# Optimization experiments

Hardware: AMD Instinct MI355X
Metric: run time of the kernel (lower is better)

Reference implementation:

```python
import jax, jax.numpy as jnp
import numpy as np

N, D, H, E = 4096, 512, 8, 131072
DH = D // H
BN_EPS = 1e-5


def setup_inputs() -> dict:
    key = jax.random.key(0)
    ks = jax.random.split(key, 12)
    def w(k, shape):
        return jax.random.normal(k, shape, dtype=jnp.float32) * 0.02
    return {
        'x': jax.random.normal(ks[0], (N, D), dtype=jnp.float32),
        'edge_index': jax.random.randint(ks[1], (2, E), 0, N),
        'edge_attr': jax.random.normal(ks[2], (E, D), dtype=jnp.float32),
        # GINE MLP: Linear(D,D) -> ReLU -> Linear(D,D)  (torch layout [out,in])
        'w_gin1': w(ks[3], (D, D)), 'b_gin1': jnp.zeros((D,), jnp.float32),
        'w_gin2': w(ks[4], (D, D)), 'b_gin2': jnp.zeros((D,), jnp.float32),
        # MultiheadAttention in/out projections
        'w_qkv': w(ks[5], (3 * D, D)), 'b_qkv': jnp.zeros((3 * D,), jnp.float32),
        'w_o': w(ks[6], (D, D)), 'b_o': jnp.zeros((D,), jnp.float32),
        # BatchNorm affine params
        'bn1l_g': jnp.ones((D,), jnp.float32), 'bn1l_b': jnp.zeros((D,), jnp.float32),
        'bn1a_g': jnp.ones((D,), jnp.float32), 'bn1a_b': jnp.zeros((D,), jnp.float32),
        # FFN: D -> 2D -> D
        'w_ff1': w(ks[7], (2 * D, D)), 'b_ff1': jnp.zeros((2 * D,), jnp.float32),
        'w_ff2': w(ks[8], (D, 2 * D)), 'b_ff2': jnp.zeros((D,), jnp.float32),
        'bn2_g': jnp.ones((D,), jnp.float32), 'bn2_b': jnp.zeros((D,), jnp.float32),
    }


def _bn(x, g, b):
    # BatchNorm1d in training mode: batch statistics over the node dim
    m = jnp.mean(x, axis=0)
    v = jnp.var(x, axis=0)
    return (x - m) * jax.lax.rsqrt(v + BN_EPS) * g + b


def _forward(x, edge_index, edge_attr,
             w_gin1, b_gin1, w_gin2, b_gin2,
             w_qkv, b_qkv, w_o, b_o,
             bn1l_g, bn1l_b, bn1a_g, bn1a_b,
             w_ff1, b_ff1, w_ff2, b_ff2, bn2_g, bn2_b):
    h_in = x
    src, dst = edge_index[0], edge_index[1]
    # --- local GINEConv: nn((1+eps)*x + sum_j relu(x_j + e_ji)), eps=0 ---
    msg = jax.nn.relu(x[src] + edge_attr)                       # [E, D]
    agg = jax.ops.segment_sum(msg, dst, num_segments=N)         # [N, D]
    gin_h = x + agg
    h_local = jax.nn.relu(gin_h @ w_gin1.T + b_gin1) @ w_gin2.T + b_gin2
    h_local = _bn(h_in + h_local, bn1l_g, bn1l_b)               # residual + BN
    # --- global multi-head self-attention over all nodes (single graph) ---
    qkv = x @ w_qkv.T + b_qkv                                   # [N, 3D]
    q, k, v = jnp.split(qkv, 3, axis=-1)
    q = q.reshape(N, H, DH).transpose(1, 0, 2)                  # [H, N, DH]
    k = k.reshape(N, H, DH).transpose(1, 0, 2)
    v = v.reshape(N, H, DH).transpose(1, 0, 2)
    scores = jnp.einsum('hnd,hmd->hnm', q, k) / np.float32(np.sqrt(DH))
    attn = jax.nn.softmax(scores, axis=-1)                      # [H, N, N]
    o = jnp.einsum('hnm,hmd->hnd', attn, v).transpose(1, 0, 2).reshape(N, D)
    h_attn = _bn(h_in + (o @ w_o.T + b_o), bn1a_g, bn1a_b)
    # --- combine branches + FFN block ---
    h = h_local + h_attn
    h = h + (jax.nn.relu(h @ w_ff1.T + b_ff1) @ w_ff2.T + b_ff2)
    return _bn(h, bn2_g, bn2_b)


def reference(x, edge_index, edge_attr,
              w_gin1, b_gin1, w_gin2, b_gin2,
              w_qkv, b_qkv, w_o, b_o,
              bn1l_g, bn1l_b, bn1a_g, bn1a_b,
              w_ff1, b_ff1, w_ff2, b_ff2, bn2_g, bn2_b):
    return _forward(x, edge_index, edge_attr,
                    w_gin1, b_gin1, w_gin2, b_gin2,
                    w_qkv, b_qkv, w_o, b_o,
                    bn1l_g, bn1l_b, bn1a_g, bn1a_b,
                    w_ff1, b_ff1, w_ff2, b_ff2, bn2_g, bn2_b)
```

## Files before the change

### kernel.cpp

```cpp
#include <hip/hip_runtime.h>

#define Nn 4096
#define Dd 512
#define Hh 8
#define Ee 131072
#define DEGCAP 96

typedef __attribute__((ext_vector_type(8))) short short8v;
typedef __attribute__((ext_vector_type(4))) short short4v;
typedef __attribute__((ext_vector_type(4))) float f32x4v;
typedef __attribute__((ext_vector_type(4))) unsigned short ushort4v;

__device__ __forceinline__ float bf2f(unsigned short u) {
    return __uint_as_float(((unsigned int)u) << 16);
}
__device__ __forceinline__ unsigned short f2bf(float f) {
    unsigned int u = __float_as_uint(f);
    return (unsigned short)((u + 0x7fff + ((u >> 16) & 1)) >> 16);
}
__device__ __forceinline__ void gl_lds16(const void* g, void* l) {
    __builtin_amdgcn_global_load_lds((const __attribute__((address_space(1))) void*)g,
                                     (__attribute__((address_space(3))) void*)l, 16, 0, 0);
}

struct CastJobs {
    const float* src[6];
    unsigned short* dst[6];
    int start[7];
    int* cnt;
    float* stats;
};

__global__ __launch_bounds__(256) void cast_multi(CastJobs cj) {
    int gid = blockIdx.x * 256 + threadIdx.x;
    if (gid < 4096) cj.cnt[gid] = 0;
    if (gid < 6144) cj.stats[gid] = 0.f;
    int b = blockIdx.x;
    int j = 0;
    while (b >= cj.start[j + 1]) j++;
    int off = (b - cj.start[j]) * 1024 + threadIdx.x * 4;
    f32x4v v = *(const f32x4v*)(cj.src[j] + off);
    ushort4v o;
    o.x = f2bf(v.x); o.y = f2bf(v.y); o.z = f2bf(v.z); o.w = f2bf(v.w);
    *(ushort4v*)(cj.dst[j] + off) = o;
}

__global__ __launch_bounds__(256) void edge_scatter(const int* __restrict__ ei,
                                                    int* __restrict__ cnt,
                                                    int* __restrict__ eidx) {
    int e = blockIdx.x * 256 + threadIdx.x;
    int d = ei[Ee + e];
    int pos = atomicAdd(&cnt[d], 1);
    if (pos < DEGCAP) eidx[d * DEGCAP + pos] = e;
}

__global__ __launch_bounds__(256) void gine_gather(const float* __restrict__ x,
                                                   const int* __restrict__ ei,
                                                   const float* __restrict__ ea,
                                                   const int* __restrict__ cnt,
                                                   const int* __restrict__ eidx,
                                                   unsigned short* __restrict__ gh,
                                                   unsigned short* __restrict__ xb) {
    __shared__ int se[DEGCAP];
    __shared__ int ss[DEGCAP];
    __shared__ float part[512];
    const int node = blockIdx.x;
    const int t = threadIdx.x;
    const int deg = min(cnt[node], DEGCAP);
    const int tc = t & 127, ep = t >> 7;

    if (t < deg) {
        int e = eidx[node * DEGCAP + t];
        se[t] = e;
        ss[t] = ei[e];
    }
    __syncthreads();

    f32x4v acc = {0.f, 0.f, 0.f, 0.f};
    int k = ep;
    while (k + 2 < deg) {
        int e0 = se[k], s0 = ss[k];
        int e1 = se[k + 2], s1 = ss[k + 2];
        f32x4v ev0 = *(const f32x4v*)(ea + (size_t)e0 * Dd + tc * 4);
        f32x4v xv0 = *(const f32x4v*)(x + (size_t)s0 * Dd + tc * 4);
        f32x4v ev1 = *(const f32x4v*)(ea + (size_t)e1 * Dd + tc * 4);
        f32x4v xv1 = *(const f32x4v*)(x + (size_t)s1 * Dd + tc * 4);
#pragma unroll
        for (int i = 0; i < 4; i++) {
            acc[i] += fmaxf(xv0[i] + ev0[i], 0.f);
            acc[i] += fmaxf(xv1[i] + ev1[i], 0.f);
        }
        k += 4;
    }
    if (k < deg) {
        int e0 = se[k], s0 = ss[k];
        f32x4v ev0 = *(const f32x4v*)(ea + (size_t)e0 * Dd + tc * 4);
        f32x4v xv0 = *(const f32x4v*)(x + (size_t)s0 * Dd + tc * 4);
#pragma unroll
        for (int i = 0; i < 4; i++) acc[i] += fmaxf(xv0[i] + ev0[i], 0.f);
    }

    if (ep) *(f32x4v*)&part[tc * 4] = acc;
    __syncthreads();
    if (!ep) {
        f32x4v o = *(const f32x4v*)&part[tc * 4];
        f32x4v xd = *(const f32x4v*)(x + (size_t)node * Dd + tc * 4);
        ushort4v ov, xv;
#pragma unroll
        for (int i = 0; i < 4; i++) {
            ov[i] = f2bf(xd[i] + acc[i] + o[i]);
            xv[i] = f2bf(xd[i]);
        }
        *(ushort4v*)(gh + (size_t)node * Dd + tc * 4) = ov;
        *(ushort4v*)(xb + (size_t)node * Dd + tc * 4) = xv;
    }
}

template <int K, int MB, bool RELU, bool OUTBF16, bool ADDRES, bool SXADD, int SOFF>
__global__ __launch_bounds__(256) void gemm_bt(const short* __restrict__ A,
                                               const short* __restrict__ B,
                                               const float* __restrict__ bias,
                                               const float* __restrict__ res,
                                               void* __restrict__ outp, int Nc,
                                               const float* __restrict__ sx,
                                               float* __restrict__ stats) {
    constexpr int BM = MB * 32;
    __shared__ alignas(16) short lA[BM * 32];
    __shared__ alignas(16) short lB[128 * 32];
    const int t = threadIdx.x;
    const int lane = t & 63, w = t >> 6;
    const int wr = w >> 1, wc = w & 1;
    const int l15 = lane & 15, lhi = lane >> 4;
    const int m0 = blockIdx.y * BM, n0 = blockIdx.x * 128;
    f32x4v acc[MB][4] = {};
    const int c0 = t, c1 = t + 256;

    for (int k0 = 0; k0 < K; k0 += 32) {
        __syncthreads();
        gl_lds16(A + (size_t)(m0 + (c0 >> 2)) * K + k0 + (c0 & 3) * 8, (char*)lA + c0 * 16);
        if constexpr (MB == 4)
            gl_lds16(A + (size_t)(m0 + (c1 >> 2)) * K + k0 + (c1 & 3) * 8, (char*)lA + c1 * 16);
        gl_lds16(B + (size_t)(n0 + (c0 >> 2)) * K + k0 + (c0 & 3) * 8, (char*)lB + c0 * 16);
        gl_lds16(B + (size_t)(n0 + (c1 >> 2)) * K + k0 + (c1 & 3) * 8, (char*)lB + c1 * 16);
        __syncthreads();
        short8v af[MB], bf[4];
#pragma unroll
        for (int m = 0; m < MB; m++)
            af[m] = *(const short8v*)&lA[(wr * (MB * 16) + m * 16 + l15) * 32 + lhi * 8];
#pragma unroll
        for (int n = 0; n < 4; n++)
            bf[n] = *(const short8v*)&lB[(wc * 64 + n * 16 + l15) * 32 + lhi * 8];
#pragma unroll
        for (int m = 0; m < MB; m++)
#pragma unroll
            for (int n = 0; n < 4; n++)
                acc[m][n] = __builtin_amdgcn_mfma_f32_16x16x32_bf16(af[m], bf[n], acc[m][n], 0, 0, 0);
    }

    float csum[4] = {0.f, 0.f, 0.f, 0.f}, cssq[4] = {0.f, 0.f, 0.f, 0.f};

#pragma unroll
    for (int m = 0; m < MB; m++)
#pragma unroll
        for (int n = 0; n < 4; n++)
#pragma unroll
            for (int j = 0; j < 4; j++) {
                int col = n0 + wc * 64 + n * 16 + l15;
                int row = m0 + wr * (MB * 16) + m * 16 + lhi * 4 + j;
                size_t idx = (size_t)row * Nc + col;
                float v = acc[m][n][j] + bias[col];
                if (RELU) v = fmaxf(v, 0.f);
                if (ADDRES) v += res[idx];
                if constexpr (SOFF >= 0) {
                    float a = SXADD ? (sx[idx] + v) : v;
                    csum[n] += a;
                    cssq[n] += a * a;
                }
                if (OUTBF16)
                    ((unsigned short*)outp)[idx] = f2bf(v);
                else
                    ((float*)outp)[idx] = v;
            }

    if constexpr (SOFF >= 0) {
        __shared__ float sst[256];
        sst[t] = 0.f;
        __syncthreads();
#pragma unroll
        for (int n = 0; n < 4; n++) {
            float s = csum[n], q = cssq[n];
            s += __shfl_xor(s, 16); s += __shfl_xor(s, 32);
            q += __shfl_xor(q, 16); q += __shfl_xor(q, 32);
            if (lhi == 0) {
                int c = wc * 64 + n * 16 + l15;
                atomicAdd(&sst[c * 2], s);
                atomicAdd(&sst[c * 2 + 1], q);
            }
        }
        __syncthreads();
        int c = t >> 1;
        atomicAdd(&stats[SOFF + (t & 1) * 512 + n0 + c], sst[t]);
    }
}

__global__ __launch_bounds__(256) void attn_fwd(const short* __restrict__ qkv,
                                                unsigned short* __restrict__ opart0,
                                                unsigned short* __restrict__ opart1,
                                                float* __restrict__ lsum) {
    __shared__ alignas(16) short lK[2][64 * 64];
    __shared__ alignas(16) short lV[2][4 * 64 * 16];
    __shared__ alignas(16) short lP[4 * 2 * 16 * 64];
    const int t = threadIdx.x, lane = t & 63, w = t >> 6;
    const int h = blockIdx.y >> 1, half = blockIdx.y & 1;
    const int kvbase = half * 2048;
    const int qw = blockIdx.x * 128 + w * 32;
    const int l15 = lane & 15, lhi = lane >> 4;
    const int ksw = l15 & 7;
    const int qs3 = (l15 >> 1) & 7;
    unsigned short* __restrict__ opart = half ? opart1 : opart0;

    short* pP = lP + w * 2048;

    short8v qf[2][2];
#pragma unroll
    for (int g = 0; g < 2; g++)
#pragma unroll
        for (int kk = 0; kk < 2; kk++)
            qf[g][kk] = *(const short8v*)&qkv[(size_t)(qw + g * 16 + l15) * 1536 + h * 64 + kk * 32 + lhi * 8];

    f32x4v oacc[2][4] = {};
    float lrow[2] = {0.f, 0.f};
    const float SC2 = 0.125f * 1.44269504f;

    int kidx[4][2];
#pragma unroll
    for (int r = 0; r < 4; r++)
#pragma unroll
        for (int kk = 0; kk < 2; kk++)
            kidx[r][kk] = (l15 + r * 16) * 64 + (((kk * 4 + lhi) ^ ksw) * 8);

    int pw_idx[4], prd_idx[2];
#pragma unroll
    for (int c2 = 0; c2 < 4; c2++)
        pw_idx[c2] = l15 * 64 + (((c2 * 2 + (lhi >> 1)) ^ qs3) * 8) + ((lhi & 1) * 4);
#pragma unroll
    for (int c = 0; c < 2; c++)
        prd_idx[c] = l15 * 64 + (((c * 4 + lhi) ^ qs3) * 8);

    unsigned vbase0 = (unsigned)(unsigned long long)&lV[0][0] + lhi * 256 + l15 * 2;

    auto stage = [&](int kt, int b) {
        int kv0 = kvbase + kt * 64;
#pragma unroll
        for (int i = 0; i < 2; i++) {
            int row = (t >> 3) + 32 * i;
            gl_lds16(qkv + (size_t)(kv0 + row) * 1536 + 512 + h * 64 + ((t & 7) ^ ((t >> 3) & 7)) * 8,
                     (char*)&lK[b][0] + t * 16 + i * 4096);
        }
#pragma unroll
        for (int i = 0; i < 2; i++) {
            int db = (t >> 7) + 2 * i;
            int kv = (t >> 1) & 63;
            int dh_in = (t & 1) * 8;
            gl_lds16(qkv + (size_t)(kv0 + kv) * 1536 + 1024 + h * 64 + db * 16 + dh_in,
                     (char*)&lV[b][0] + t * 16 + i * 4096);
        }
    };

    stage(0, 0);
    __syncthreads();

    for (int kt = 0; kt < 32; kt++) {
        const int b = kt & 1;
        if (kt + 1 < 32) stage(kt + 1, b ^ 1);

        const short* Kb = &lK[b][0];
        const unsigned vbase = vbase0 + b * 8192;

        f32x4v s0[4] = {}, s1[4] = {};
        __builtin_amdgcn_s_setprio(1);
#pragma unroll
        for (int r = 0; r < 4; r++) {
            short8v k0 = *(const short8v*)&Kb[kidx[r][0]];
            short8v k1 = *(const short8v*)&Kb[kidx[r][1]];
            s0[r] = __builtin_amdgcn_mfma_f32_16x16x32_bf16(k0, qf[0][0], s0[r], 0, 0, 0);
            s0[r] = __builtin_amdgcn_mfma_f32_16x16x32_bf16(k1, qf[0][1], s0[r], 0, 0, 0);
            s1[r] = __builtin_amdgcn_mfma_f32_16x16x32_bf16(k0, qf[1][0], s1[r], 0, 0, 0);
            s1[r] = __builtin_amdgcn_mfma_f32_16x16x32_bf16(k1, qf[1][1], s1[r], 0, 0, 0);
        }
        __builtin_amdgcn_s_setprio(0);

#pragma unroll
        for (int g = 0; g < 2; g++) {
            f32x4v* s = g ? s1 : s0;
            float p[16];
            float rs = 0.f;
#pragma unroll
            for (int r = 0; r < 4; r++)
#pragma unroll
                for (int j = 0; j < 4; j++) {
                    float e = exp2f(fmaf(s[r][j], SC2, -4.f));
                    p[r * 4 + j] = e;
                    rs += e;
                }
            rs += __shfl_xor(rs, 16);
            rs += __shfl_xor(rs, 32);
            lrow[g] += rs;

            short* pPg = pP + g * 1024;
#pragma unroll
            for (int c2 = 0; c2 < 4; c2++) {
                short4v pk;
#pragma unroll
                for (int j = 0; j < 4; j++) pk[j] = (short)f2bf(p[c2 * 4 + j]);
                *(short4v*)&pPg[pw_idx[c2]] = pk;
            }
        }
        asm volatile("" ::: "memory");

        short8v pf[2][2];
#pragma unroll
        for (int g = 0; g < 2; g++)
#pragma unroll
            for (int c = 0; c < 2; c++)
                pf[g][c] = *(const short8v*)&pP[g * 1024 + prd_idx[c]];

        short4v v00a, v00b, v01a, v01b, v10a, v10b, v11a, v11b;
        short4v v20a, v20b, v21a, v21b, v30a, v30b, v31a, v31b;
        asm volatile("ds_read_b64_tr_b16 %0, %1" : "=v"(v00a) : "v"(vbase));
        asm volatile("ds_read_b64_tr_b16 %0, %1 offset:128" : "=v"(v00b) : "v"(vbase));
        asm volatile("ds_read_b64_tr_b16 %0, %1 offset:1024" : "=v"(v01a) : "v"(vbase));
        asm volatile("ds_read_b64_tr_b16 %0, %1 offset:1152" : "=v"(v01b) : "v"(vbase));
        asm volatile("ds_read_b64_tr_b16 %0, %1 offset:2048" : "=v"(v10a) : "v"(vbase));
        asm volatile("ds_read_b64_tr_b16 %0, %1 offset:2176" : "=v"(v10b) : "v"(vbase));
        asm volatile("ds_read_b64_tr_b16 %0, %1 offset:3072" : "=v"(v11a) : "v"(vbase));
        asm volatile("ds_read_b64_tr_b16 %0, %1 offset:3200" : "=v"(v11b) : "v"(vbase));
        asm volatile("ds_read_b64_tr_b16 %0, %1 offset:4096" : "=v"(v20a) : "v"(vbase));
        asm volatile("ds_read_b64_tr_b16 %0, %1 offset:4224" : "=v"(v20b) : "v"(vbase));
        asm volatile("ds_read_b64_tr_b16 %0, %1 offset:5120" : "=v"(v21a) : "v"(vbase));
        asm volatile("ds_read_b64_tr_b16 %0, %1 offset:5248" : "=v"(v21b) : "v"(vbase));
        asm volatile("ds_read_b64_tr_b16 %0, %1 offset:6144" : "=v"(v30a) : "v"(vbase));
        asm volatile("ds_read_b64_tr_b16 %0, %1 offset:6272" : "=v"(v30b) : "v"(vbase));
        asm volatile("ds_read_b64_tr_b16 %0, %1 offset:7168" : "=v"(v31a) : "v"(vbase));
        asm volatile("ds_read_b64_tr_b16 %0, %1 offset:7296" : "=v"(v31b) : "v"(vbase));

        asm volatile("s_waitcnt lgkmcnt(0)" ::: "memory");
        __builtin_amdgcn_sched_barrier(0);

#define VFCAT(a, b) __builtin_shufflevector(a, b, 0, 1, 2, 3, 4, 5, 6, 7)
        short8v vv[4][2];
        vv[0][0] = VFCAT(v00a, v00b); vv[0][1] = VFCAT(v01a, v01b);
        vv[1][0] = VFCAT(v10a, v10b); vv[1][1] = VFCAT(v11a, v11b);
        vv[2][0] = VFCAT(v20a, v20b); vv[2][1] = VFCAT(v21a, v21b);
        vv[3][0] = VFCAT(v30a, v30b); vv[3][1] = VFCAT(v31a, v31b);
#undef VFCAT
        __builtin_amdgcn_s_setprio(1);
#pragma unroll
        for (int g = 0; g < 2; g++)
#pragma unroll
            for (int n = 0; n < 4; n++) {
                oacc[g][n] = __builtin_amdgcn_mfma_f32_16x16x32_bf16(pf[g][0], vv[n][0], oacc[g][n], 0, 0, 0);
                oacc[g][n] = __builtin_amdgcn_mfma_f32_16x16x32_bf16(pf[g][1], vv[n][1], oacc[g][n], 0, 0, 0);
            }
        __builtin_amdgcn_s_setprio(0);

        __syncthreads();
    }

#pragma unroll
    for (int g = 0; g < 2; g++) {
#pragma unroll
        for (int j = 0; j < 4; j++) {
            int row = qw + g * 16 + lhi * 4 + j;
#pragma unroll
            for (int n = 0; n < 4; n++)
                opart[(size_t)row * Dd + h * 64 + n * 16 + l15] = f2bf(oacc[g][n][j]);
        }
        if (lhi == 0)
            lsum[(size_t)(half * Hh + h) * Nn + qw + g * 16 + l15] = lrow[g];
    }
}

__global__ __launch_bounds__(256) void attn_combine(const unsigned short* __restrict__ o0,
                                                    const unsigned short* __restrict__ o1,
                                                    const float* __restrict__ lsum,
                                                    unsigned short* __restrict__ ob) {
    int idx = (blockIdx.x * 256 + threadIdx.x) * 4;
    int row = idx >> 9, col = idx & 511, h = col >> 6;
    float l0 = lsum[(size_t)h * Nn + row];
    float l1 = lsum[(size_t)(Hh + h) * Nn + row];
    float inv = 1.f / (l0 + l1);
    ushort4v n1 = *(const ushort4v*)(o0 + idx);
    ushort4v n2 = *(const ushort4v*)(o1 + idx);
    ushort4v o;
#pragma unroll
    for (int e = 0; e < 4; e++)
        o[e] = f2bf((bf2f(n1[e]) + bf2f(n2[e])) * inv);
    *(ushort4v*)(ob + idx) = o;
}

__global__ __launch_bounds__(256) void bn_combine(const float* __restrict__ x,
                                                  const float* __restrict__ p1,
                                                  const float* __restrict__ p2,
                                                  const float* __restrict__ stats,
                                                  const float* __restrict__ g1,
                                                  const float* __restrict__ b1,
                                                  const float* __restrict__ g2,
                                                  const float* __restrict__ b2,
                                                  float* __restrict__ h,
                                                  unsigned short* __restrict__ hb) {
    int i0 = (blockIdx.x * 256 + threadIdx.x) * 4;
    int c0 = i0 & 511;
    f32x4v xv = *(const f32x4v*)(x + i0);
    f32x4v av = *(const f32x4v*)(p1 + i0);
    f32x4v bv = *(const f32x4v*)(p2 + i0);
    f32x4v hv;
    ushort4v hbv;
#pragma unroll
    for (int e = 0; e < 4; e++) {
        int c = c0 + e;
        float ma = stats[c] * (1.f / Nn);
        float va = stats[512 + c] * (1.f / Nn) - ma * ma;
        float sA = g1[c] * rsqrtf(va + 1e-5f);
        float bA = b1[c] - ma * sA;
        float mb = stats[1024 + c] * (1.f / Nn);
        float vb = stats[1536 + c] * (1.f / Nn) - mb * mb;
        float sB = g2[c] * rsqrtf(vb + 1e-5f);
        float bB = b2[c] - mb * sB;
        float a = xv[e] + av[e];
        float b = xv[e] + bv[e];
        float val = a * sA + bA + b * sB + bB;
        hv[e] = val;
        hbv[e] = f2bf(val);
    }
    *(f32x4v*)(h + i0) = hv;
    *(ushort4v*)(hb + i0) = hbv;
}

__global__ __launch_bounds__(256) void bn_apply(float* __restrict__ out,
                                                const float* __restrict__ stats,
                                                const float* __restrict__ g,
                                                const float* __restrict__ b) {
    int i0 = (blockIdx.x * 256 + threadIdx.x) * 4;
    int c0 = i0 & 511;
    f32x4v v = *(const f32x4v*)(out + i0);
#pragma unroll
    for (int e = 0; e < 4; e++) {
        int c = c0 + e;
        float m = stats[4096 + c] * (1.f / Nn);
        float va = stats[4608 + c] * (1.f / Nn) - m * m;
        float s = g[c] * rsqrtf(va + 1e-5f);
        v[e] = (v[e] - m) * s + b[c];
    }
    *(f32x4v*)(out + i0) = v;
}

extern "C" void kernel_launch(void* const* d_in, const int* in_sizes, int n_in,
                              void* d_out, int out_size, void* d_ws, size_t ws_size,
                              hipStream_t stream) {
    const float* x = (const float*)d_in[0];
    const int* ei = (const int*)d_in[1];
    const float* ea = (const float*)d_in[2];
    const float* w_gin1 = (const float*)d_in[3];
    const float* b_gin1 = (const float*)d_in[4];
    const float* w_gin2 = (const float*)d_in[5];
    const float* b_gin2 = (const float*)d_in[6];
    const float* w_qkv = (const float*)d_in[7];
    const float* b_qkv = (const float*)d_in[8];
    const float* w_o = (const float*)d_in[9];
    const float* b_o = (const float*)d_in[10];
    const float* bn1l_g = (const float*)d_in[11];
    const float* bn1l_b = (const float*)d_in[12];
    const float* bn1a_g = (const float*)d_in[13];
    const float* bn1a_b = (const float*)d_in[14];
    const float* w_ff1 = (const float*)d_in[15];
    const float* b_ff1 = (const float*)d_in[16];
    const float* w_ff2 = (const float*)d_in[17];
    const float* b_ff2 = (const float*)d_in[18];
    const float* bn2_g = (const float*)d_in[19];
    const float* bn2_b = (const float*)d_in[20];

    char* ws = (char*)d_ws;
    unsigned short* wg1b = (unsigned short*)(ws + 0);
    unsigned short* wg2b = (unsigned short*)(ws + 524288);
    unsigned short* wqkvb = (unsigned short*)(ws + 1048576);
    unsigned short* wob = (unsigned short*)(ws + 2621440);
    unsigned short* wf1b = (unsigned short*)(ws + 3145728);
    unsigned short* wf2b = (unsigned short*)(ws + 4194304);
    unsigned short* xb = (unsigned short*)(ws + 5242880);
    unsigned short* qkvb = (unsigned short*)(ws + 9437184);
    int* eidx = (int*)(ws + 22020096);
    int* cnt = (int*)(ws + 23592960);
    unsigned short* ginh = (unsigned short*)(ws + 30408704);
    float* lsum = (float*)(ws + 30408704);
    unsigned short* t1 = (unsigned short*)(ws + 34603008);
    float* hlp = (float*)(ws + 38797312);
    unsigned short* obuf = (unsigned short*)(ws + 47185920);
    float* attn_pre = (float*)(ws + 51380224);
    float* hbuf = (float*)(ws + 59768832);
    unsigned short* opart0 = (unsigned short*)(ws + 59768832);
    unsigned short* hb = (unsigned short*)(ws + 68157440);
    unsigned short* t2 = (unsigned short*)(ws + 72351744);
    unsigned short* opart1 = (unsigned short*)(ws + 72351744);
    float* stats = (float*)(ws + 80740352);

    CastJobs cj;
    cj.src[0] = w_gin1; cj.dst[0] = wg1b;
    cj.src[1] = w_gin2; cj.dst[1] = wg2b;
    cj.src[2] = w_qkv;  cj.dst[2] = wqkvb;
    cj.src[3] = w_o;    cj.dst[3] = wob;
    cj.src[4] = w_ff1;  cj.dst[4] = wf1b;
    cj.src[5] = w_ff2;  cj.dst[5] = wf2b;
    cj.cnt = cnt;
    cj.stats = stats;
    int nelem[6] = {Dd * Dd, Dd * Dd, 3 * Dd * Dd, Dd * Dd, 2 * Dd * Dd, 2 * Dd * Dd};
    cj.start[0] = 0;
    for (int i = 0; i < 6; i++) cj.start[i + 1] = cj.start[i] + nelem[i] / 1024;
    cast_multi<<<cj.start[6], 256, 0, stream>>>(cj);

    edge_scatter<<<Ee / 256, 256, 0, stream>>>(ei, cnt, eidx);
    gine_gather<<<Nn, 256, 0, stream>>>(x, ei, ea, cnt, eidx, ginh, xb);

    gemm_bt<512, 2, true, true, false, false, -1><<<dim3(4, 64), 256, 0, stream>>>(
        (const short*)ginh, (const short*)wg1b, b_gin1, nullptr, t1, 512, nullptr, nullptr);
    gemm_bt<512, 2, false, false, false, true, 0><<<dim3(4, 64), 256, 0, stream>>>(
        (const short*)t1, (const short*)wg2b, b_gin2, nullptr, hlp, 512, x, stats);

    gemm_bt<512, 4, false, true, false, false, -1><<<dim3(12, 32), 256, 0, stream>>>(
        (const short*)xb, (const short*)wqkvb, b_qkv, nullptr, qkvb, 1536, nullptr, nullptr);
    attn_fwd<<<dim3(Nn / 128, Hh * 2), 256, 0, stream>>>((const short*)qkvb, opart0, opart1, lsum);
    attn_combine<<<Nn * Dd / 1024, 256, 0, stream>>>(opart0, opart1, lsum, obuf);
    gemm_bt<512, 2, false, false, false, true, 1024><<<dim3(4, 64), 256, 0, stream>>>(
        (const short*)obuf, (const short*)wob, b_o, nullptr, attn_pre, 512, x, stats);

    bn_combine<<<Nn * Dd / 1024, 256, 0, stream>>>(x, hlp, attn_pre, stats,
                                                   bn1l_g, bn1l_b, bn1a_g, bn1a_b, hbuf, hb);

    gemm_bt<512, 4, true, true, false, false, -1><<<dim3(8, 32), 256, 0, stream>>>(
        (const short*)hb, (const short*)wf1b, b_ff1, nullptr, t2, 1024, nullptr, nullptr);
    gemm_bt<1024, 2, false, false, true, false, 4096><<<dim3(4, 64), 256, 0, stream>>>(
        (const short*)t2, (const short*)wf2b, b_ff2, hbuf, d_out, 512, nullptr, stats);

    bn_apply<<<Nn * Dd / 1024, 256, 0, stream>>>((float*)d_out, stats, bn2_g, bn2_b);
}
```

Measured before the change: 280.8 us.

## Merge independent GEMMs and attention into shared launches, fuse attention combine into O-proj

Turns the GEMM and attention kernels into device bodies that take explicit shared memory, then launches independent work together. GIN linear1 runs with the QKV projection, and GIN linear2 runs with the attention kernel, so each pair fills the GPU from a single grid. The attention split-combine (sum of the two halves divided by the softmax denominators) moves into the A-tile load of the output-projection GEMM, which removes a separate kernel and the obuf round trip. The costs are that the combine now uses plain global loads instead of async LDS loads and is recomputed for each of the four column tiles. The combined grids also share one smem size, which may lower occupancy for the GEMM blocks placed in the attention launch.

```diff
diff --git a/kernel.cpp b/kernel.cpp
--- a/kernel.cpp
+++ b/kernel.cpp
@@ -7,6 +7,7 @@
 #define DEGCAP 96
 
 typedef __attribute__((ext_vector_type(8))) short short8v;
+typedef __attribute__((ext_vector_type(8))) unsigned short ushort8v;
 typedef __attribute__((ext_vector_type(4))) short short4v;
 typedef __attribute__((ext_vector_type(4))) float f32x4v;
 typedef __attribute__((ext_vector_type(4))) unsigned short ushort4v;
@@ -116,30 +117,49 @@
     }
 }
 
-template <int K, int MB, bool RELU, bool OUTBF16, bool ADDRES, bool SXADD, int SOFF>
-__global__ __launch_bounds__(256) void gemm_bt(const short* __restrict__ A,
-                                               const short* __restrict__ B,
-                                               const float* __restrict__ bias,
-                                               const float* __restrict__ res,
-                                               void* __restrict__ outp, int Nc,
-                                               const float* __restrict__ sx,
-                                               float* __restrict__ stats) {
+template <int K, int MB, bool RELU, bool OUTBF16, bool ADDRES, bool SXADD, int SOFF, bool ACOMB>
+__device__ __forceinline__ void gemm_body(char* smem,
+                                          const short* __restrict__ A,
+                                          const short* __restrict__ B,
+                                          const float* __restrict__ bias,
+                                          const float* __restrict__ res,
+                                          void* __restrict__ outp, int Nc,
+                                          const float* __restrict__ sx,
+                                          float* __restrict__ stats,
+                                          const unsigned short* __restrict__ op0,
+                                          const unsigned short* __restrict__ op1,
+                                          const float* __restrict__ lsum,
+                                          int bx, int by, int t) {
     constexpr int BM = MB * 32;
-    __shared__ alignas(16) short lA[BM * 32];
-    __shared__ alignas(16) short lB[128 * 32];
-    const int t = threadIdx.x;
+    short* lA = (short*)smem;
+    short* lB = (short*)(smem + MB * 2048);
+    float* sst = (float*)(smem + MB * 2048 + 8192);
     const int lane = t & 63, w = t >> 6;
     const int wr = w >> 1, wc = w & 1;
     const int l15 = lane & 15, lhi = lane >> 4;
-    const int m0 = blockIdx.y * BM, n0 = blockIdx.x * 128;
+    const int m0 = by * BM, n0 = bx * 128;
     f32x4v acc[MB][4] = {};
     const int c0 = t, c1 = t + 256;
 
     for (int k0 = 0; k0 < K; k0 += 32) {
         __syncthreads();
-        gl_lds16(A + (size_t)(m0 + (c0 >> 2)) * K + k0 + (c0 & 3) * 8, (char*)lA + c0 * 16);
-        if constexpr (MB == 4)
-            gl_lds16(A + (size_t)(m0 + (c1 >> 2)) * K + k0 + (c1 & 3) * 8, (char*)lA + c1 * 16);
+        if constexpr (ACOMB) {
+            int r = c0 >> 2, s = c0 & 3;
+            int row = m0 + r;
+            int kb = k0 + s * 8;
+            int h = k0 >> 6;
+            float inv = 1.f / (lsum[(size_t)h * Nn + row] + lsum[(size_t)(Hh + h) * Nn + row]);
+            ushort8v p0 = *(const ushort8v*)&op0[(size_t)row * 512 + kb];
+            ushort8v p1 = *(const ushort8v*)&op1[(size_t)row * 512 + kb];
+            short8v ov;
+#pragma unroll
+            for (int i = 0; i < 8; i++) ov[i] = (short)f2bf((bf2f(p0[i]) + bf2f(p1[i])) * inv);
+            *(short8v*)((char*)lA + c0 * 16) = ov;
+        } else {
+            gl_lds16(A + (size_t)(m0 + (c0 >> 2)) * K + k0 + (c0 & 3) * 8, (char*)lA + c0 * 16);
+            if constexpr (MB == 4)
+                gl_lds16(A + (size_t)(m0 + (c1 >> 2)) * K + k0 + (c1 & 3) * 8, (char*)lA + c1 * 16);
+        }
         gl_lds16(B + (size_t)(n0 + (c0 >> 2)) * K + k0 + (c0 & 3) * 8, (char*)lB + c0 * 16);
         gl_lds16(B + (size_t)(n0 + (c1 >> 2)) * K + k0 + (c1 & 3) * 8, (char*)lB + c1 * 16);
         __syncthreads();
@@ -183,7 +203,6 @@
             }
 
     if constexpr (SOFF >= 0) {
-        __shared__ float sst[256];
         sst[t] = 0.f;
         __syncthreads();
 #pragma unroll
@@ -198,28 +217,25 @@
             }
         }
         __syncthreads();
-        int c = t >> 1;
-        atomicAdd(&stats[SOFF + (t & 1) * 512 + n0 + c], sst[t]);
-    }
-}
-
-__global__ __launch_bounds__(256) void attn_fwd(const short* __restrict__ qkv,
-                                                unsigned short* __restrict__ opart0,
-                                                unsigned short* __restrict__ opart1,
-                                                float* __restrict__ lsum) {
-    __shared__ alignas(16) short lK[2][64 * 64];
-    __shared__ alignas(16) short lV[2][4 * 64 * 16];
-    __shared__ alignas(16) short lP[4 * 2 * 16 * 64];
-    const int t = threadIdx.x, lane = t & 63, w = t >> 6;
-    const int h = blockIdx.y >> 1, half = blockIdx.y & 1;
+        atomicAdd(&stats[SOFF + (t & 1) * 512 + n0 + (t >> 1)], sst[t]);
+    }
+}
+
+__device__ __forceinline__ void attn_body(char* smem, const short* __restrict__ qkv,
+                                          unsigned short* __restrict__ opart0,
+                                          unsigned short* __restrict__ opart1,
+                                          float* __restrict__ lsum,
+                                          int bx, int by, int t) {
+    const int lane = t & 63, w = t >> 6;
+    const int h = by >> 1, half = by & 1;
     const int kvbase = half * 2048;
-    const int qw = blockIdx.x * 128 + w * 32;
+    const int qw = bx * 128 + w * 32;
     const int l15 = lane & 15, lhi = lane >> 4;
     const int ksw = l15 & 7;
     const int qs3 = (l15 >> 1) & 7;
     unsigned short* __restrict__ opart = half ? opart1 : opart0;
 
-    short* pP = lP + w * 2048;
+    short* pP = (short*)(smem + 32768) + w * 2048;
 
     short8v qf[2][2];
 #pragma unroll
@@ -247,15 +263,14 @@
     for (int c = 0; c < 2; c++)
         prd_idx[c] = l15 * 64 + (((c * 4 + lhi) ^ qs3) * 8);
 
-    unsigned vbase0 = (unsigned)(unsigned long long)&lV[0][0] + lhi * 256 + l15 * 2;
+    unsigned vbase0 = (unsigned)(size_t)(smem + 16384) + lhi * 256 + l15 * 2;
 
     auto stage = [&](int kt, int b) {
         int kv0 = kvbase + kt * 64;
 #pragma unroll
         for (int i = 0; i < 2; i++) {
-            int row = (t >> 3) + 32 * i;
-            gl_lds16(qkv + (size_t)(kv0 + row) * 1536 + 512 + h * 64 + ((t & 7) ^ ((t >> 3) & 7)) * 8,
-                     (char*)&lK[b][0] + t * 16 + i * 4096);
+            gl_lds16(qkv + (size_t)(kv0 + (t >> 3) + 32 * i) * 1536 + 512 + h * 64 + ((t & 7) ^ ((t >> 3) & 7)) * 8,
+                     smem + b * 8192 + t * 16 + i * 4096);
         }
 #pragma unroll
         for (int i = 0; i < 2; i++) {
@@ -263,7 +278,7 @@
             int kv = (t >> 1) & 63;
             int dh_in = (t & 1) * 8;
             gl_lds16(qkv + (size_t)(kv0 + kv) * 1536 + 1024 + h * 64 + db * 16 + dh_in,
-                     (char*)&lV[b][0] + t * 16 + i * 4096);
+                     smem + 16384 + b * 8192 + t * 16 + i * 4096);
         }
     };
 
@@ -274,7 +289,7 @@
         const int b = kt & 1;
         if (kt + 1 < 32) stage(kt + 1, b ^ 1);
 
-        const short* Kb = &lK[b][0];
+        const short* Kb = (const short*)smem + b * 4096;
         const unsigned vbase = vbase0 + b * 8192;
 
         f32x4v s0[4] = {}, s1[4] = {};
@@ -381,22 +396,67 @@
     }
 }
 
-__global__ __launch_bounds__(256) void attn_combine(const unsigned short* __restrict__ o0,
-                                                    const unsigned short* __restrict__ o1,
-                                                    const float* __restrict__ lsum,
-                                                    unsigned short* __restrict__ ob) {
-    int idx = (blockIdx.x * 256 + threadIdx.x) * 4;
-    int row = idx >> 9, col = idx & 511, h = col >> 6;
-    float l0 = lsum[(size_t)h * Nn + row];
-    float l1 = lsum[(size_t)(Hh + h) * Nn + row];
-    float inv = 1.f / (l0 + l1);
-    ushort4v n1 = *(const ushort4v*)(o0 + idx);
-    ushort4v n2 = *(const ushort4v*)(o1 + idx);
-    ushort4v o;
-#pragma unroll
-    for (int e = 0; e < 4; e++)
-        o[e] = f2bf((bf2f(n1[e]) + bf2f(n2[e])) * inv);
-    *(ushort4v*)(ob + idx) = o;
+__global__ __launch_bounds__(256) void gin1_qkv(const short* ginh, const short* wg1b,
+                                                const float* b_gin1, unsigned short* t1,
+                                                const short* xb, const short* wqkvb,
+                                                const float* b_qkv, unsigned short* qkvb) {
+    __shared__ char smem[16384];
+    int b = blockIdx.x, t = threadIdx.x;
+    if (b < 256) {
+        gemm_body<512, 2, true, true, false, false, -1, false>(
+            smem, ginh, wg1b, b_gin1, nullptr, t1, 512, nullptr, nullptr,
+            nullptr, nullptr, nullptr, b & 3, b >> 2, t);
+    } else {
+        int bb = b - 256;
+        gemm_body<512, 4, false, true, false, false, -1, false>(
+            smem, xb, wqkvb, b_qkv, nullptr, qkvb, 1536, nullptr, nullptr,
+            nullptr, nullptr, nullptr, bb % 12, bb / 12, t);
+    }
+}
+
+__global__ __launch_bounds__(256) void gin2_attn(const short* qkvb, unsigned short* op0,
+                                                 unsigned short* op1, float* lsum,
+                                                 const short* t1, const short* wg2b,
+                                                 const float* b_gin2, float* hlp,
+                                                 const float* x, float* stats) {
+    __shared__ char smem[49152];
+    int b = blockIdx.x, t = threadIdx.x;
+    if (b < 512) {
+        attn_body(smem, qkvb, op0, op1, lsum, b & 31, b >> 5, t);
+    } else {
+        int bb = b - 512;
+        gemm_body<512, 2, false, false, false, true, 0, false>(
+            smem, t1, wg2b, b_gin2, nullptr, hlp, 512, x, stats,
+            nullptr, nullptr, nullptr, bb & 3, bb >> 2, t);
+    }
+}
+
+__global__ __launch_bounds__(256) void oproj_fused(const short* wob, const float* b_o,
+                                                   float* attn_pre, const float* x, float* stats,
+                                                   const unsigned short* op0,
+                                                   const unsigned short* op1,
+                                                   const float* lsum) {
+    __shared__ char smem[13312];
+    gemm_body<512, 2, false, false, false, true, 1024, true>(
+        smem, nullptr, wob, b_o, nullptr, attn_pre, 512, x, stats,
+        op0, op1, lsum, blockIdx.x, blockIdx.y, threadIdx.x);
+}
+
+__global__ __launch_bounds__(256) void ff1_k(const short* hb, const short* wf1b,
+                                             const float* b_ff1, unsigned short* t2) {
+    __shared__ char smem[16384];
+    gemm_body<512, 4, true, true, false, false, -1, false>(
+        smem, hb, wf1b, b_ff1, nullptr, t2, 1024, nullptr, nullptr,
+        nullptr, nullptr, nullptr, blockIdx.x, blockIdx.y, threadIdx.x);
+}
+
+__global__ __launch_bounds__(256) void ff2_k(const short* t2, const short* wf2b,
+                                             const float* b_ff2, const float* hbuf,
+                                             float* dout, float* stats) {
+    __shared__ char smem[13312];
+    gemm_body<1024, 2, false, false, true, false, 4096, false>(
+        smem, t2, wf2b, b_ff2, hbuf, dout, 512, nullptr, stats,
+        nullptr, nullptr, nullptr, blockIdx.x, blockIdx.y, threadIdx.x);
 }
 
 __global__ __launch_bounds__(256) void bn_combine(const float* __restrict__ x,
@@ -495,7 +555,6 @@
     float* lsum = (float*)(ws + 30408704);
     unsigned short* t1 = (unsigned short*)(ws + 34603008);
     float* hlp = (float*)(ws + 38797312);
-    unsigned short* obuf = (unsigned short*)(ws + 47185920);
     float* attn_pre = (float*)(ws + 51380224);
     float* hbuf = (float*)(ws + 59768832);
     unsigned short* opart0 = (unsigned short*)(ws + 59768832);
@@ -521,25 +580,22 @@
     edge_scatter<<<Ee / 256, 256, 0, stream>>>(ei, cnt, eidx);
     gine_gather<<<Nn, 256, 0, stream>>>(x, ei, ea, cnt, eidx, ginh, xb);
 
-    gemm_bt<512, 2, true, true, false, false, -1><<<dim3(4, 64), 256, 0, stream>>>(
-        (const short*)ginh, (const short*)wg1b, b_gin1, nullptr, t1, 512, nullptr, nullptr);
-    gemm_bt<512, 2, false, false, false, true, 0><<<dim3(4, 64), 256, 0, stream>>>(
-        (const short*)t1, (const short*)wg2b, b_gin2, nullptr, hlp, 512, x, stats);
-
-    gemm_bt<512, 4, false, true, false, false, -1><<<dim3(12, 32), 256, 0, stream>>>(
-        (const short*)xb, (const short*)wqkvb, b_qkv, nullptr, qkvb, 1536, nullptr, nullptr);
-    attn_fwd<<<dim3(Nn / 128, Hh * 2), 256, 0, stream>>>((const short*)qkvb, opart0, opart1, lsum);
-    attn_combine<<<Nn * Dd / 1024, 256, 0, stream>>>(opart0, opart1, lsum, obuf);
-    gemm_bt<512, 2, false, false, false, true, 1024><<<dim3(4, 64), 256, 0, stream>>>(
-        (const short*)obuf, (const short*)wob, b_o, nullptr, attn_pre, 512, x, stats);
+    gin1_qkv<<<640, 256, 0, stream>>>((const short*)ginh, (const short*)wg1b, b_gin1, t1,
+                                      (const short*)xb, (const short*)wqkvb, b_qkv, qkvb);
+
+    gin2_attn<<<768, 256, 0, stream>>>((const short*)qkvb, opart0, opart1, lsum,
+                                       (const short*)t1, (const short*)wg2b, b_gin2, hlp,
+                                       x, stats);
+
+    oproj_fused<<<dim3(4, 64), 256, 0, stream>>>((const short*)wob, b_o, attn_pre, x, stats,
+                                                 opart0, opart1, lsum);
 
     bn_combine<<<Nn * Dd / 1024, 256, 0, stream>>>(x, hlp, attn_pre, stats,
                                                    bn1l_g, bn1l_b, bn1a_g, bn1a_b, hbuf, hb);
 
-    gemm_bt<512, 4, true, true, false, false, -1><<<dim3(8, 32), 256, 0, stream>>>(
-        (const short*)hb, (const short*)wf1b, b_ff1, nullptr, t2, 1024, nullptr, nullptr);
-    gemm_bt<1024, 2, false, false, true, false, 4096><<<dim3(4, 64), 256, 0, stream>>>(
-        (const short*)t2, (const short*)wf2b, b_ff2, hbuf, d_out, 512, nullptr, stats);
+    ff1_k<<<dim3(8, 32), 256, 0, stream>>>((const short*)hb, (const short*)wf1b, b_ff1, t2);
+    ff2_k<<<dim3(4, 64), 256, 0, stream>>>((const short*)t2, (const short*)wf2b, b_ff2,
+                                           hbuf, (float*)d_out, stats);
 
     bn_apply<<<Nn * Dd / 1024, 256, 0, stream>>>((float*)d_out, stats, bn2_g, bn2_b);
 }
```

Measured after the change: 260.6 us. 7.2% less time.
